# Kernel tuning notes

Hardware: AMD Instinct MI355X
Metric: run time of the kernel (lower is better)

Reference implementation:

```python
import jax, jax.numpy as jnp
import numpy as np

O_IDX = 0  # slot_types.index('O')
X_IDX = 1  # slot_types.index('X')
NUM_INTENTS = 60
NUM_SLOTS = 100
ENCODER_DIM = 300
COS_EPS = 1e-8  # torch CosineSimilarity eps


def _l2_normalize(x):
    n = jnp.linalg.norm(x, axis=-1, keepdims=True)
    return x / jnp.maximum(n, COS_EPS)


def _ce_on_probs(probs, labels):
    # torch cross_entropy applied to (already softmaxed) probs as logits
    logz = jax.nn.logsumexp(probs, axis=-1)
    picked = jnp.take_along_axis(probs, labels[..., None], axis=-1)[..., 0]
    return logz - picked


def setup_inputs() -> dict:
    key = jax.random.key(0)
    ks = jax.random.split(key, 12)
    B, T, H = 128, 128, 768
    inp = {
        'lm_output_1': jax.random.normal(ks[0], (B, T, H), jnp.float32),
        'lm_output_2': jax.random.normal(ks[1], (B, T, H), jnp.float32),
        'intent_labels_1': jax.random.randint(ks[2], (B,), 0, NUM_INTENTS, jnp.int32),
        'intent_labels_2': jax.random.randint(ks[3], (B,), 0, NUM_INTENTS, jnp.int32),
        'slot_labels_1': jax.random.randint(ks[4], (B, T), 0, NUM_SLOTS, jnp.int32),
        'slot_labels_2': jax.random.randint(ks[5], (B, T), 0, NUM_SLOTS, jnp.int32),
        'intent_proto_in': jax.random.normal(ks[6], (NUM_INTENTS, ENCODER_DIM), jnp.float32),
        'intent_count_in': jax.random.randint(ks[7], (NUM_INTENTS,), 1, 50, jnp.int32),
        'slot_proto_in': jax.random.normal(ks[8], (NUM_SLOTS, H), jnp.float32),
        'slot_count_in': jax.random.randint(ks[9], (NUM_SLOTS,), 1, 50, jnp.int32),
        'W_enc': jax.random.normal(ks[10], (ENCODER_DIM, H), jnp.float32) * 0.02,
        'b_enc': jax.random.normal(ks[11], (ENCODER_DIM,), jnp.float32) * 0.02,
        'b_O': jnp.zeros(()),
        'b_X': jnp.zeros(()),
    }
    return inp


def reference(lm_output_1, lm_output_2, intent_labels_1, intent_labels_2,
              slot_labels_1, slot_labels_2, intent_proto_in, intent_count_in,
              slot_proto_in, slot_count_in, W_enc, b_enc, b_O, b_X):
    B, T, H = lm_output_1.shape
    # encoder Linear(hidden -> 300); dropout is identity in eval mode
    enc1 = lm_output_1 @ W_enc.T + b_enc   # [B,T,E]
    enc2 = lm_output_2 @ W_enc.T + b_enc   # [B,T,E] == decoded_2 (use_aae=False)
    slot_proto_enc = slot_proto_in @ W_enc.T + b_enc  # [S,E]

    # ---- prototype update: segment-mean of batch-1 embeddings by class ----
    cls1 = enc1[:, 0, :]  # [B,E]
    i_sum = jax.ops.segment_sum(cls1, intent_labels_1, num_segments=NUM_INTENTS)
    i_cnt = jax.ops.segment_sum(jnp.ones((B,), jnp.float32), intent_labels_1,
                                num_segments=NUM_INTENTS)
    cnt0 = intent_count_in.astype(jnp.float32)
    intent_proto = (cnt0[:, None] * intent_proto_in + i_sum) / (cnt0 + i_cnt)[:, None]
    # faithful to original bug: new count = mean-vector dim = encoder_dim
    intent_count = jnp.full((NUM_INTENTS,), ENCODER_DIM, jnp.int32)

    toks1 = enc1[:, 1:, :].reshape(B * (T - 1), -1)       # [B*(T-1),E]
    slab1 = slot_labels_1[:, 1:].reshape(-1)
    s_sum = jax.ops.segment_sum(toks1, slab1, num_segments=NUM_SLOTS)
    s_cnt = jax.ops.segment_sum(jnp.ones_like(slab1, dtype=jnp.float32), slab1,
                                num_segments=NUM_SLOTS)
    scnt0 = slot_count_in.astype(jnp.float32)
    slot_proto = (scnt0[:, None] * slot_proto_enc + s_sum) / (scnt0 + s_cnt)[:, None]
    slot_count = slot_count_in + s_cnt.astype(jnp.int32)

    # ---- intent: cosine sim to prototypes, softmax, CE on the softmax output ----
    cls2 = enc2[:, 0, :]  # [B,E]
    intent_sim = _l2_normalize(cls2) @ _l2_normalize(intent_proto).T  # [B,I]
    intent_probs = jax.nn.softmax(intent_sim, axis=-1)
    intent_logits = intent_probs[:, None, :]  # [B,1,I]
    intent_loss = jnp.mean(_ce_on_probs(intent_probs, intent_labels_2))

    # ---- slots: cosine sim per token, O/X columns are detached biases ----
    toks2 = enc2[:, 1:, :]  # [B,T-1,E]
    slot_sim = jnp.einsum('btd,sd->bts', _l2_normalize(toks2), _l2_normalize(slot_proto))
    slot_sim = slot_sim.at[:, :, O_IDX].set(jax.lax.stop_gradient(b_O))
    slot_sim = slot_sim.at[:, :, X_IDX].set(jax.lax.stop_gradient(b_X))
    slot_probs = jax.nn.softmax(slot_sim, axis=-1)  # [B,T-1,S]
    slot_logits = slot_probs[:, :, None, :]  # [B,T-1,1,S]
    slot_loss = jnp.mean(_ce_on_probs(slot_probs, slot_labels_2[:, 1:]))

    total_loss = intent_loss + slot_loss
    return (intent_logits, slot_logits, intent_loss, slot_loss, total_loss,
            intent_proto, intent_count, slot_proto, slot_count)
```

## Files before the change

### kernel.cpp

```cpp
#include <hip/hip_runtime.h>
#include <math.h>

#define BB_ 128
#define TT_ 128
#define HDIM 768
#define ED 300
#define NI 60
#define NS 100
#define NTOK 16256

#define WS_ENC1  0
#define WS_ENC2  4915200
#define WS_SPE   9830400
#define WS_ISUM  9860400
#define WS_ICNT  9878400
#define WS_NPTI  9878464
#define WS_NPTS  9896464
#define WS_SSUM  9926464
#define WS_SCNT  9956464
#define WS_PART  9956608
#define WS_LOSSI 13779328
#define WS_LOSSS 13779456

#define O_ILOG   0
#define O_SLOG   7680
#define O_ILOSS  1633280
#define O_SLOSS  1633281
#define O_TLOSS  1633282
#define O_IPROTO 1633283
#define O_ICNT   1651283
#define O_SPROTO 1651343
#define O_SCNT   1681343

typedef __attribute__((ext_vector_type(8))) __bf16 bf16x8;
typedef __attribute__((ext_vector_type(4))) float f32x4;

__device__ __forceinline__ unsigned bf16_rne_u(float x) {
  unsigned u = __float_as_uint(x);
  return (u + 0x7FFFu + ((u >> 16) & 1u)) >> 16;
}
__device__ __forceinline__ void split2(float x, float y, unsigned& hi, unsigned& lo) {
  unsigned hx = bf16_rne_u(x), hy = bf16_rne_u(y);
  float rx = x - __uint_as_float(hx << 16);
  float ry = y - __uint_as_float(hy << 16);
  unsigned lx = bf16_rne_u(rx), ly = bf16_rne_u(ry);
  hi = hx | (hy << 16);
  lo = lx | (ly << 16);
}

__device__ __forceinline__ void gl_lds16(const uint4* g, void* l) {
  __builtin_amdgcn_global_load_lds(
      (const __attribute__((address_space(1))) void*)g,
      (__attribute__((address_space(3))) void*)l, 16, 0, 0);
}

__global__ __launch_bounds__(256) void prep_w(const float* __restrict__ W,
                                              uint4* __restrict__ Wp) {
  int t = blockIdx.x * 256 + threadIdx.x;
  if (t >= 30720) return;
  int ks  = t / 1280;
  int rem = t - ks * 1280;
  int nf  = rem >> 6;
  int c   = (rem >> 2) & 15;
  int kg  = rem & 3;
  int n   = nf * 16 + c;
  int kb  = ks * 32 + kg * 8;
  float4 x0 = make_float4(0.f, 0.f, 0.f, 0.f), x1 = x0;
  if (n < 300) {
    x0 = *(const float4*)(W + (size_t)n * HDIM + kb);
    x1 = *(const float4*)(W + (size_t)n * HDIM + kb + 4);
  }
  unsigned h0, l0, h1, l1, h2, l2, h3, l3;
  split2(x0.x, x0.y, h0, l0); split2(x0.z, x0.w, h1, l1);
  split2(x1.x, x1.y, h2, l2); split2(x1.z, x1.w, h3, l3);
  size_t base = (size_t)ks * 2560;
  int slot = nf * 64 + kg * 16 + c;
  Wp[base + slot]        = make_uint4(h0, h1, h2, h3);
  Wp[base + 1280 + slot] = make_uint4(l0, l1, l2, l3);
}

__global__ __launch_bounds__(512, 4) void gemm_enc_mfma(
    const float* __restrict__ lm1, const float* __restrict__ lm2,
    const float* __restrict__ spin, const uint4* __restrict__ Wp,
    const float* __restrict__ bias, float* __restrict__ ws) {
  __shared__ __align__(16) unsigned char smem[49152];
  int mt = blockIdx.x, m0 = mt * 64;
  const float* src; int srow, mrows;
  if (mt < 256)      { src = lm1;  srow = m0;         mrows = 64; }
  else if (mt < 512) { src = lm2;  srow = m0 - 16384; mrows = 64; }
  else               { src = spin; srow = m0 - 32768; mrows = 100 - srow; }

  int tid = threadIdx.x;
  int l = tid & 63, w = tid >> 6;
  int mf = w & 3, nh = w >> 2;

  int ar = tid >> 3, a8 = tid & 7;
  bool aval = ar < mrows;
  const float* aptr = src + (size_t)(srow + ar) * HDIM + a8 * 4;
  unsigned aw = 40960u + ((unsigned)(ar >> 4) << 10) + ((unsigned)(a8 >> 1) << 8)
              + ((unsigned)(ar & 15) << 4) + ((unsigned)(a8 & 1) << 3);

  const unsigned char* arop = smem + 40960 + (mf << 10) + l * 16;
  const unsigned char* brop = smem + ((nh * 10) << 10) + l * 16;

  f32x4 acc[10];
  #pragma unroll
  for (int i = 0; i < 10; i++) acc[i] = (f32x4)0.f;

  float4 areg = aval ? *(const float4*)(aptr) : make_float4(0.f, 0.f, 0.f, 0.f);

  for (int ks = 0; ks < 24; ks++) {
    {
      unsigned h0, l0, h1, l1;
      split2(areg.x, areg.y, h0, l0);
      split2(areg.z, areg.w, h1, l1);
      *(uint2*)(smem + aw)        = make_uint2(h0, h1);
      *(uint2*)(smem + aw + 4096) = make_uint2(l0, l1);
    }
    {
      const uint4* gp = Wp + (size_t)ks * 2560 + (size_t)(w * 5) * 64 + l;
      #pragma unroll
      for (int i = 0; i < 5; i++)
        gl_lds16(gp + i * 64, smem + (w * 5 + i) * 1024);
    }
    __syncthreads();
    if (ks < 23)
      areg = aval ? *(const float4*)(aptr + (ks + 1) * 32)
                  : make_float4(0.f, 0.f, 0.f, 0.f);
    bf16x8 ah = *(const bf16x8*)(arop);
    bf16x8 al = *(const bf16x8*)(arop + 4096);
    #pragma unroll
    for (int nf = 0; nf < 10; nf++) {
      bf16x8 bh = *(const bf16x8*)(brop + (nf << 10));
      bf16x8 bl = *(const bf16x8*)(brop + (nf << 10) + 20480);
      acc[nf] = __builtin_amdgcn_mfma_f32_16x16x32_bf16(ah, bh, acc[nf], 0, 0, 0);
      acc[nf] = __builtin_amdgcn_mfma_f32_16x16x32_bf16(al, bh, acc[nf], 0, 0, 0);
      acc[nf] = __builtin_amdgcn_mfma_f32_16x16x32_bf16(ah, bl, acc[nf], 0, 0, 0);
    }
    __syncthreads();
  }

  int rbase = (mf << 4) + ((l >> 4) << 2);
  #pragma unroll
  for (int nf = 0; nf < 10; nf++) {
    int n = ((nh * 10 + nf) << 4) + (l & 15);
    if (n >= 300) continue;
    float bn = bias[n];
    #pragma unroll
    for (int r = 0; r < 4; r++) {
      int lr = rbase + r;
      if (lr < mrows) ws[(size_t)(m0 + lr) * ED + n] = acc[nf][r] + bn;
    }
  }
}

__global__ __launch_bounds__(320) void intent_seg(
    const float* __restrict__ enc1, const int* __restrict__ il1,
    float* __restrict__ isum, float* __restrict__ icnt) {
  int seg = blockIdx.x, tid = threadIdx.x;
  if (tid < ED) {
    float a = 0.f;
    for (int b = 0; b < BB_; b++)
      if (il1[b] == seg) a += enc1[(size_t)(b * TT_) * ED + tid];
    isum[seg * ED + tid] = a;
  } else if (tid == ED) {
    float c = 0.f;
    for (int b = 0; b < BB_; b++) c += (il1[b] == seg) ? 1.f : 0.f;
    icnt[seg] = c;
  }
}

__global__ __launch_bounds__(320) void slot_seg_partial(
    const float* __restrict__ enc1, const int* __restrict__ sl1,
    float* __restrict__ part) {
  __shared__ float acc[15050];
  int gid = blockIdx.x;
  int g = gid >> 1, h = gid & 1;
  int tid = threadIdx.x;
  for (int i = tid; i < 15050; i += 320) acc[i] = 0.f;
  __syncthreads();
  int base = h * 50;
  for (int rr = 0; rr < 128; rr++) {
    int j = g * 128 + rr;
    int bb = j / 127, tt = j % 127 + 1;
    int l = sl1[bb * TT_ + tt] - base;
    if (l >= 0 && l < 50) {
      if (tid < ED)       acc[l * ED + tid] += enc1[(size_t)(bb * TT_ + tt) * ED + tid];
      else if (tid == ED) acc[15000 + l] += 1.f;
    }
  }
  __syncthreads();
  float* dst = part + (size_t)gid * 15050;
  for (int i = tid; i < 15050; i += 320) dst[i] = acc[i];
}

__global__ void slot_seg_final(const float* __restrict__ part,
                               float* __restrict__ ssum, float* __restrict__ scnt) {
  int idx = blockIdx.x * 256 + threadIdx.x;
  if (idx < 30000) {
    int S = idx / ED, d = idx % ED;
    int h = S / 50, ls = S % 50;
    float a = 0.f;
    for (int g = 0; g < 127; g++) a += part[(size_t)(g * 2 + h) * 15050 + ls * ED + d];
    ssum[idx] = a;
  } else if (idx < 30100) {
    int S = idx - 30000;
    int h = S / 50, ls = S % 50;
    float a = 0.f;
    for (int g = 0; g < 127; g++) a += part[(size_t)(g * 2 + h) * 15050 + 15000 + ls];
    scnt[S] = a;
  }
}

__global__ void finalize_protos(
    const float* __restrict__ ipin, const int* __restrict__ icin,
    const float* __restrict__ spe, const int* __restrict__ scin,
    const float* __restrict__ isum, const float* __restrict__ icnt,
    const float* __restrict__ ssum, const float* __restrict__ scnt,
    float* __restrict__ dout) {
  int idx = blockIdx.x * 256 + threadIdx.x;
  if (idx < 18000) {
    int i = idx / ED;
    float c0 = (float)icin[i];
    dout[O_IPROTO + idx] = (c0 * ipin[idx] + isum[idx]) / (c0 + icnt[i]);
  } else if (idx < 18060) {
    dout[O_ICNT + (idx - 18000)] = (float)ED;
  } else if (idx < 48060) {
    int k = idx - 18060;
    int s = k / ED;
    float c0 = (float)scin[s];
    dout[O_SPROTO + k] = (c0 * spe[k] + ssum[k]) / (c0 + scnt[s]);
  } else if (idx < 48160) {
    int s = idx - 48060;
    dout[O_SCNT + s] = (float)scin[s] + scnt[s];
  }
}

__global__ __launch_bounds__(320) void norm_protos(
    const float* __restrict__ dout, float* __restrict__ ws) {
  int row = blockIdx.x;
  const float* src; float* dstT; int nrows; int r;
  if (row < NI) { r = row;      src = dout + O_IPROTO + (size_t)r * ED; dstT = ws + WS_NPTI; nrows = NI; }
  else          { r = row - NI; src = dout + O_SPROTO + (size_t)r * ED; dstT = ws + WS_NPTS; nrows = NS; }
  int tid = threadIdx.x;
  float v = (tid < ED) ? src[tid] : 0.f;
  float ss = v * v;
  #pragma unroll
  for (int o = 32; o > 0; o >>= 1) ss += __shfl_xor(ss, o);
  __shared__ float wsum[5];
  if ((tid & 63) == 0) wsum[tid >> 6] = ss;
  __syncthreads();
  float tot = wsum[0] + wsum[1] + wsum[2] + wsum[3] + wsum[4];
  float den = fmaxf(sqrtf(tot), 1e-8f);
  if (tid < ED) dstT[(size_t)tid * nrows + r] = v / den;
}

__global__ __launch_bounds__(64) void intent_head(
    const float* __restrict__ enc2, const float* __restrict__ npTi,
    const int* __restrict__ il2, float* __restrict__ dout,
    float* __restrict__ lossi) {
  int b = blockIdx.x;
  __shared__ float row[ED];
  int tid = threadIdx.x;
  const float* src = enc2 + (size_t)(b * TT_) * ED;
  float ss = 0.f;
  for (int k = tid; k < ED; k += 64) { float v = src[k]; row[k] = v; ss += v * v; }
  #pragma unroll
  for (int o = 32; o > 0; o >>= 1) ss += __shfl_xor(ss, o);
  __syncthreads();
  float den = fmaxf(sqrtf(ss), 1e-8f);
  float dot = 0.f;
  if (tid < NI)
    for (int k = 0; k < ED; k++) dot = fmaf(row[k], npTi[k * NI + tid], dot);
  float sim = dot / den;
  float val = (tid < NI) ? sim : -INFINITY;
  float m = val;
  #pragma unroll
  for (int o = 32; o > 0; o >>= 1) m = fmaxf(m, __shfl_xor(m, o));
  float e = (tid < NI) ? expf(sim - m) : 0.f;
  float s = e;
  #pragma unroll
  for (int o = 32; o > 0; o >>= 1) s += __shfl_xor(s, o);
  float prob = e / s;
  if (tid < NI) dout[O_ILOG + b * NI + tid] = prob;
  float pv = (tid < NI) ? prob : -INFINITY;
  float m2 = pv;
  #pragma unroll
  for (int o = 32; o > 0; o >>= 1) m2 = fmaxf(m2, __shfl_xor(m2, o));
  float e2 = (tid < NI) ? expf(prob - m2) : 0.f;
  float s2 = e2;
  #pragma unroll
  for (int o = 32; o > 0; o >>= 1) s2 += __shfl_xor(s2, o);
  int lbl = il2[b];
  float picked = __shfl(prob, lbl);
  if (tid == 0) lossi[b] = m2 + logf(s2) - picked;
}

__device__ __forceinline__ float bsum128(float v, float* red2) {
  #pragma unroll
  for (int o = 32; o > 0; o >>= 1) v += __shfl_xor(v, o);
  __syncthreads();
  if ((threadIdx.x & 63) == 0) red2[threadIdx.x >> 6] = v;
  __syncthreads();
  return red2[0] + red2[1];
}
__device__ __forceinline__ float bmax128(float v, float* red2) {
  #pragma unroll
  for (int o = 32; o > 0; o >>= 1) v = fmaxf(v, __shfl_xor(v, o));
  __syncthreads();
  if ((threadIdx.x & 63) == 0) red2[threadIdx.x >> 6] = v;
  __syncthreads();
  return fmaxf(red2[0], red2[1]);
}

#define RPB 8
__global__ __launch_bounds__(128) void slot_head(
    const float* __restrict__ enc2, const float* __restrict__ npTs,
    const int* __restrict__ sl2, const float* __restrict__ bO,
    const float* __restrict__ bX, float* __restrict__ dout,
    float* __restrict__ losss) {
  __shared__ float rows[RPB][ED];
  __shared__ float den[RPB];
  __shared__ float red2[2];
  __shared__ float pickedS;
  int tid = threadIdx.x;
  int jb = blockIdx.x * RPB;
  for (int idx = tid; idx < RPB * ED; idx += 128) {
    int r = idx / ED, k = idx % ED;
    int j = jb + r;
    int bb = j / 127, tt = j % 127 + 1;
    rows[r][k] = enc2[(size_t)(bb * TT_ + tt) * ED + k];
  }
  __syncthreads();
  #pragma unroll
  for (int r = 0; r < RPB; r++) {
    float ss = 0.f;
    for (int k = tid; k < ED; k += 128) { float v = rows[r][k]; ss += v * v; }
    ss = bsum128(ss, red2);
    if (tid == 0) den[r] = fmaxf(sqrtf(ss), 1e-8f);
  }
  __syncthreads();
  float acc[RPB] = {};
  int p = tid;
  bool act = p < NS;
  for (int k = 0; k < ED; k += 4) {
    float w0 = act ? npTs[(size_t)(k + 0) * NS + p] : 0.f;
    float w1 = act ? npTs[(size_t)(k + 1) * NS + p] : 0.f;
    float w2 = act ? npTs[(size_t)(k + 2) * NS + p] : 0.f;
    float w3 = act ? npTs[(size_t)(k + 3) * NS + p] : 0.f;
    #pragma unroll
    for (int r = 0; r < RPB; r++) {
      float4 rv = *(const float4*)&rows[r][k];
      acc[r] = fmaf(rv.x, w0, acc[r]);
      acc[r] = fmaf(rv.y, w1, acc[r]);
      acc[r] = fmaf(rv.z, w2, acc[r]);
      acc[r] = fmaf(rv.w, w3, acc[r]);
    }
  }
  float vO = *bO, vX = *bX;
  for (int r = 0; r < RPB; r++) {
    int j = jb + r;
    int bb = j / 127, tt = j % 127 + 1;
    float sim = acc[r] / den[r];
    if (p == 0) sim = vO;
    if (p == 1) sim = vX;
    float val = act ? sim : -INFINITY;
    float m = bmax128(val, red2);
    float e = act ? expf(sim - m) : 0.f;
    float s = bsum128(e, red2);
    float prob = e / s;
    if (act) dout[O_SLOG + (size_t)j * NS + p] = prob;
    float pv = act ? prob : -INFINITY;
    float m2 = bmax128(pv, red2);
    int lbl = sl2[bb * TT_ + tt];
    if (p == lbl) pickedS = prob;
    float e2 = act ? expf(prob - m2) : 0.f;
    float s2 = bsum128(e2, red2);
    if (tid == 0) losss[j] = m2 + logf(s2) - pickedS;
  }
}

__global__ __launch_bounds__(256) void loss_final(
    const float* __restrict__ li, const float* __restrict__ lsv,
    float* __restrict__ dout) {
  __shared__ float red[256];
  int tid = threadIdx.x;
  float a = (tid < BB_) ? li[tid] : 0.f;
  red[tid] = a;
  __syncthreads();
  for (int o = 128; o > 0; o >>= 1) {
    if (tid < o) red[tid] += red[tid + o];
    __syncthreads();
  }
  float il = red[0];
  __syncthreads();
  float bsum = 0.f;
  for (int i = tid; i < NTOK; i += 256) bsum += lsv[i];
  red[tid] = bsum;
  __syncthreads();
  for (int o = 128; o > 0; o >>= 1) {
    if (tid < o) red[tid] += red[tid + o];
    __syncthreads();
  }
  if (tid == 0) {
    float ilm = il / 128.f;
    float slm = red[0] / 16256.f;
    dout[O_ILOSS] = ilm;
    dout[O_SLOSS] = slm;
    dout[O_TLOSS] = ilm + slm;
  }
}

extern "C" void kernel_launch(void* const* d_in, const int* in_sizes, int n_in,
                              void* d_out, int out_size, void* d_ws, size_t ws_size,
                              hipStream_t stream) {
  const float* lm1  = (const float*)d_in[0];
  const float* lm2  = (const float*)d_in[1];
  const int*   il1  = (const int*)d_in[2];
  const int*   il2  = (const int*)d_in[3];
  const int*   sl1  = (const int*)d_in[4];
  const int*   sl2  = (const int*)d_in[5];
  const float* ipin = (const float*)d_in[6];
  const int*   icin = (const int*)d_in[7];
  const float* spin = (const float*)d_in[8];
  const int*   scin = (const int*)d_in[9];
  const float* W    = (const float*)d_in[10];
  const float* benc = (const float*)d_in[11];
  const float* bO   = (const float*)d_in[12];
  const float* bX   = (const float*)d_in[13];
  float* out = (float*)d_out;
  float* ws  = (float*)d_ws;
  uint4* Wp  = (uint4*)(ws + WS_PART);

  prep_w<<<120, 256, 0, stream>>>(W, Wp);
  gemm_enc_mfma<<<514, 512, 0, stream>>>(lm1, lm2, spin, Wp, benc, ws);
  intent_seg<<<60, 320, 0, stream>>>(ws + WS_ENC1, il1, ws + WS_ISUM, ws + WS_ICNT);
  slot_seg_partial<<<254, 320, 0, stream>>>(ws + WS_ENC1, sl1, ws + WS_PART);
  slot_seg_final<<<118, 256, 0, stream>>>(ws + WS_PART, ws + WS_SSUM, ws + WS_SCNT);
  finalize_protos<<<189, 256, 0, stream>>>(ipin, icin, ws + WS_SPE, scin,
                                           ws + WS_ISUM, ws + WS_ICNT,
                                           ws + WS_SSUM, ws + WS_SCNT, out);
  norm_protos<<<160, 320, 0, stream>>>(out, ws);
  intent_head<<<128, 64, 0, stream>>>(ws + WS_ENC2, ws + WS_NPTI, il2, out, ws + WS_LOSSI);
  slot_head<<<2032, 128, 0, stream>>>(ws + WS_ENC2, ws + WS_NPTS, sl2, bO, bX, out, ws + WS_LOSSS);
  loss_final<<<1, 256, 0, stream>>>(ws + WS_LOSSI, ws + WS_LOSSS, out);
}
```

Before: 369.5 us.

## Compute slot cosine similarities with split-bf16 MFMA instead of scalar FMA

Replaces the scalar per-thread slot_head with an MFMA kernel. Normalised token rows are split into bf16 hi/lo pairs and multiplied against pre-packed, split normalised slot prototypes using three 16x16x32 bf16 MFMAs per tile, giving near-fp32 accuracy. A new prep_npts kernel packs the prototype matrix into the MFMA-friendly layout, reusing the WS_PART workspace. The softmax and CE reductions now run per 16-lane group with shuffles, replacing block-wide syncthreads reductions, and each block handles 32 tokens. The cost is an extra launch and a small precision loss from the bf16x3 decomposition.

```diff
diff --git a/kernel.cpp b/kernel.cpp
--- a/kernel.cpp
+++ b/kernel.cpp
@@ -255,6 +255,30 @@
   if (tid < ED) dstT[(size_t)tid * nrows + r] = v / den;
 }
 
+__global__ __launch_bounds__(256) void prep_npts(const float* __restrict__ npTs,
+                                                 uint4* __restrict__ Wq) {
+  int t = blockIdx.x * 256 + threadIdx.x;
+  if (t >= 4480) return;
+  int ks  = t / 448;
+  int rem = t - ks * 448;
+  int nf  = rem >> 6;
+  int c   = (rem >> 2) & 15;
+  int kg  = rem & 3;
+  int s   = nf * 16 + c;
+  int kb  = ks * 32 + kg * 8;
+  float v[8];
+  #pragma unroll
+  for (int i = 0; i < 8; i++)
+    v[i] = (s < NS && (kb + i) < ED) ? npTs[(size_t)(kb + i) * NS + s] : 0.f;
+  unsigned h0, l0, h1, l1, h2, l2, h3, l3;
+  split2(v[0], v[1], h0, l0); split2(v[2], v[3], h1, l1);
+  split2(v[4], v[5], h2, l2); split2(v[6], v[7], h3, l3);
+  size_t base = (size_t)ks * 896;
+  int slot = nf * 64 + kg * 16 + c;
+  Wq[base + slot]       = make_uint4(h0, h1, h2, h3);
+  Wq[base + 448 + slot] = make_uint4(l0, l1, l2, l3);
+}
+
 __global__ __launch_bounds__(64) void intent_head(
     const float* __restrict__ enc2, const float* __restrict__ npTi,
     const int* __restrict__ il2, float* __restrict__ dout,
@@ -296,87 +320,149 @@
   if (tid == 0) lossi[b] = m2 + logf(s2) - picked;
 }
 
-__device__ __forceinline__ float bsum128(float v, float* red2) {
-  #pragma unroll
-  for (int o = 32; o > 0; o >>= 1) v += __shfl_xor(v, o);
-  __syncthreads();
-  if ((threadIdx.x & 63) == 0) red2[threadIdx.x >> 6] = v;
-  __syncthreads();
-  return red2[0] + red2[1];
-}
-__device__ __forceinline__ float bmax128(float v, float* red2) {
-  #pragma unroll
-  for (int o = 32; o > 0; o >>= 1) v = fmaxf(v, __shfl_xor(v, o));
-  __syncthreads();
-  if ((threadIdx.x & 63) == 0) red2[threadIdx.x >> 6] = v;
-  __syncthreads();
-  return fmaxf(red2[0], red2[1]);
-}
-
-#define RPB 8
-__global__ __launch_bounds__(128) void slot_head(
-    const float* __restrict__ enc2, const float* __restrict__ npTs,
+__global__ __launch_bounds__(128) void slot_head_mfma(
+    const float* __restrict__ enc2, const uint4* __restrict__ Wq,
     const int* __restrict__ sl2, const float* __restrict__ bO,
     const float* __restrict__ bX, float* __restrict__ dout,
     float* __restrict__ losss) {
-  __shared__ float rows[RPB][ED];
-  __shared__ float den[RPB];
-  __shared__ float red2[2];
-  __shared__ float pickedS;
+  __shared__ __align__(16) unsigned char smem[18560];
+  float* invd = (float*)(smem + 18432);
   int tid = threadIdx.x;
-  int jb = blockIdx.x * RPB;
-  for (int idx = tid; idx < RPB * ED; idx += 128) {
-    int r = idx / ED, k = idx % ED;
-    int j = jb + r;
-    int bb = j / 127, tt = j % 127 + 1;
-    rows[r][k] = enc2[(size_t)(bb * TT_ + tt) * ED + k];
-  }
-  __syncthreads();
-  #pragma unroll
-  for (int r = 0; r < RPB; r++) {
-    float ss = 0.f;
-    for (int k = tid; k < ED; k += 128) { float v = rows[r][k]; ss += v * v; }
-    ss = bsum128(ss, red2);
-    if (tid == 0) den[r] = fmaxf(sqrtf(ss), 1e-8f);
-  }
-  __syncthreads();
-  float acc[RPB] = {};
-  int p = tid;
-  bool act = p < NS;
-  for (int k = 0; k < ED; k += 4) {
-    float w0 = act ? npTs[(size_t)(k + 0) * NS + p] : 0.f;
-    float w1 = act ? npTs[(size_t)(k + 1) * NS + p] : 0.f;
-    float w2 = act ? npTs[(size_t)(k + 2) * NS + p] : 0.f;
-    float w3 = act ? npTs[(size_t)(k + 3) * NS + p] : 0.f;
-    #pragma unroll
-    for (int r = 0; r < RPB; r++) {
-      float4 rv = *(const float4*)&rows[r][k];
-      acc[r] = fmaf(rv.x, w0, acc[r]);
-      acc[r] = fmaf(rv.y, w1, acc[r]);
-      acc[r] = fmaf(rv.z, w2, acc[r]);
-      acc[r] = fmaf(rv.w, w3, acc[r]);
-    }
-  }
+  int l = tid & 63, w = tid >> 6;
+  int blk = blockIdx.x;
+  int j0 = blk * 32;
+
+  int nrow = tid >> 2, nq = tid & 3;
+  int jn = j0 + nrow;
+  int tokn = (jn / 127) * TT_ + (jn % 127) + 1;
+  const float* nsrc = enc2 + (size_t)tokn * ED + nq * 75;
+  float ss = 0.f;
+  for (int i = 0; i < 75; i++) { float v = nsrc[i]; ss = fmaf(v, v, ss); }
+  ss += __shfl_xor(ss, 1);
+  ss += __shfl_xor(ss, 2);
+  if (nq == 0) invd[nrow] = 1.f / fmaxf(sqrtf(ss), 1e-8f);
+  __syncthreads();
+
+  const float* asrc = enc2 + (size_t)tokn * ED;
+  unsigned awr = 14336u + ((unsigned)(nrow >> 4) << 10) + ((unsigned)nq << 8)
+               + ((unsigned)(nrow & 15) << 4);
+  float ainv = invd[nrow];
+
+  const unsigned char* arop = smem + 14336 + (w << 10) + l * 16;
+  const unsigned char* brop = smem + l * 16;
+
+  f32x4 acc[7];
+  #pragma unroll
+  for (int i = 0; i < 7; i++) acc[i] = (f32x4)0.f;
+
+  for (int ks = 0; ks < 10; ks++) {
+    {
+      int k0 = ks * 32 + nq * 8;
+      float4 v0 = (k0 <= 296) ? *(const float4*)(asrc + k0)
+                              : make_float4(0.f, 0.f, 0.f, 0.f);
+      float4 v1 = (k0 + 4 <= 296) ? *(const float4*)(asrc + k0 + 4)
+                                  : make_float4(0.f, 0.f, 0.f, 0.f);
+      v0.x *= ainv; v0.y *= ainv; v0.z *= ainv; v0.w *= ainv;
+      v1.x *= ainv; v1.y *= ainv; v1.z *= ainv; v1.w *= ainv;
+      unsigned h0, l0, h1, l1, h2, l2, h3, l3;
+      split2(v0.x, v0.y, h0, l0); split2(v0.z, v0.w, h1, l1);
+      split2(v1.x, v1.y, h2, l2); split2(v1.z, v1.w, h3, l3);
+      *(uint4*)(smem + awr)        = make_uint4(h0, h1, h2, h3);
+      *(uint4*)(smem + awr + 2048) = make_uint4(l0, l1, l2, l3);
+    }
+    {
+      const uint4* gp = Wq + (size_t)ks * 896;
+      #pragma unroll
+      for (int i = 0; i < 7; i++) {
+        int c1 = i * 2 + w;
+        gl_lds16(gp + c1 * 64 + l, smem + c1 * 1024);
+      }
+    }
+    __syncthreads();
+    bf16x8 ah = *(const bf16x8*)(arop);
+    bf16x8 al = *(const bf16x8*)(arop + 2048);
+    #pragma unroll
+    for (int nf = 0; nf < 7; nf++) {
+      bf16x8 bh = *(const bf16x8*)(brop + (nf << 10));
+      bf16x8 bl = *(const bf16x8*)(brop + (nf << 10) + 7168);
+      acc[nf] = __builtin_amdgcn_mfma_f32_16x16x32_bf16(ah, bh, acc[nf], 0, 0, 0);
+      acc[nf] = __builtin_amdgcn_mfma_f32_16x16x32_bf16(al, bh, acc[nf], 0, 0, 0);
+      acc[nf] = __builtin_amdgcn_mfma_f32_16x16x32_bf16(ah, bl, acc[nf], 0, 0, 0);
+    }
+    __syncthreads();
+  }
+
   float vO = *bO, vX = *bX;
-  for (int r = 0; r < RPB; r++) {
-    int j = jb + r;
-    int bb = j / 127, tt = j % 127 + 1;
-    float sim = acc[r] / den[r];
-    if (p == 0) sim = vO;
-    if (p == 1) sim = vX;
-    float val = act ? sim : -INFINITY;
-    float m = bmax128(val, red2);
-    float e = act ? expf(sim - m) : 0.f;
-    float s = bsum128(e, red2);
-    float prob = e / s;
-    if (act) dout[O_SLOG + (size_t)j * NS + p] = prob;
-    float pv = act ? prob : -INFINITY;
-    float m2 = bmax128(pv, red2);
-    int lbl = sl2[bb * TT_ + tt];
-    if (p == lbl) pickedS = prob;
-    float e2 = act ? expf(prob - m2) : 0.f;
-    float s2 = bsum128(e2, red2);
-    if (tid == 0) losss[j] = m2 + logf(s2) - pickedS;
+  int c16 = l & 15, g = l >> 4;
+  #pragma unroll
+  for (int r = 0; r < 4; r++) {
+    int j = j0 + w * 16 + g * 4 + r;
+    int tok = (j / 127) * TT_ + (j % 127) + 1;
+    int lbl = sl2[tok];
+    float sim[7];
+    #pragma unroll
+    for (int nf = 0; nf < 7; nf++) sim[nf] = acc[nf][r];
+    if (c16 == 0) sim[0] = vO;
+    if (c16 == 1) sim[0] = vX;
+    float mx = -INFINITY;
+    #pragma unroll
+    for (int nf = 0; nf < 7; nf++) {
+      bool valid = (nf < 6) || (c16 < 4);
+      float v = valid ? sim[nf] : -INFINITY;
+      mx = fmaxf(mx, v);
+    }
+    mx = fmaxf(mx, __shfl_xor(mx, 1));
+    mx = fmaxf(mx, __shfl_xor(mx, 2));
+    mx = fmaxf(mx, __shfl_xor(mx, 4));
+    mx = fmaxf(mx, __shfl_xor(mx, 8));
+    float e[7], s = 0.f;
+    #pragma unroll
+    for (int nf = 0; nf < 7; nf++) {
+      bool valid = (nf < 6) || (c16 < 4);
+      e[nf] = valid ? expf(sim[nf] - mx) : 0.f;
+      s += e[nf];
+    }
+    s += __shfl_xor(s, 1);
+    s += __shfl_xor(s, 2);
+    s += __shfl_xor(s, 4);
+    s += __shfl_xor(s, 8);
+    float p[7];
+    #pragma unroll
+    for (int nf = 0; nf < 7; nf++) p[nf] = e[nf] / s;
+    #pragma unroll
+    for (int nf = 0; nf < 7; nf++) {
+      int col = nf * 16 + c16;
+      if (col < NS) dout[O_SLOG + (size_t)j * NS + col] = p[nf];
+    }
+    float m2 = -INFINITY;
+    #pragma unroll
+    for (int nf = 0; nf < 7; nf++) {
+      bool valid = (nf < 6) || (c16 < 4);
+      m2 = fmaxf(m2, valid ? p[nf] : -INFINITY);
+    }
+    m2 = fmaxf(m2, __shfl_xor(m2, 1));
+    m2 = fmaxf(m2, __shfl_xor(m2, 2));
+    m2 = fmaxf(m2, __shfl_xor(m2, 4));
+    m2 = fmaxf(m2, __shfl_xor(m2, 8));
+    float s2 = 0.f, pick = 0.f;
+    #pragma unroll
+    for (int nf = 0; nf < 7; nf++) {
+      bool valid = (nf < 6) || (c16 < 4);
+      if (valid) {
+        s2 += expf(p[nf] - m2);
+        int col = nf * 16 + c16;
+        pick += (col == lbl) ? p[nf] : 0.f;
+      }
+    }
+    s2 += __shfl_xor(s2, 1);
+    s2 += __shfl_xor(s2, 2);
+    s2 += __shfl_xor(s2, 4);
+    s2 += __shfl_xor(s2, 8);
+    pick += __shfl_xor(pick, 1);
+    pick += __shfl_xor(pick, 2);
+    pick += __shfl_xor(pick, 4);
+    pick += __shfl_xor(pick, 8);
+    if (c16 == 0) losss[j] = m2 + logf(s2) - pick;
   }
 }
 
@@ -431,6 +517,7 @@
   float* out = (float*)d_out;
   float* ws  = (float*)d_ws;
   uint4* Wp  = (uint4*)(ws + WS_PART);
+  uint4* Wq  = (uint4*)(ws + WS_PART);
 
   prep_w<<<120, 256, 0, stream>>>(W, Wp);
   gemm_enc_mfma<<<514, 512, 0, stream>>>(lm1, lm2, spin, Wp, benc, ws);
@@ -442,6 +529,7 @@
                                            ws + WS_SSUM, ws + WS_SCNT, out);
   norm_protos<<<160, 320, 0, stream>>>(out, ws);
   intent_head<<<128, 64, 0, stream>>>(ws + WS_ENC2, ws + WS_NPTI, il2, out, ws + WS_LOSSI);
-  slot_head<<<2032, 128, 0, stream>>>(ws + WS_ENC2, ws + WS_NPTS, sl2, bO, bX, out, ws + WS_LOSSS);
+  prep_npts<<<18, 256, 0, stream>>>(ws + WS_NPTS, Wq);
+  slot_head_mfma<<<508, 128, 0, stream>>>(ws + WS_ENC2, Wq, sl2, bO, bX, out, ws + WS_LOSSS);
   loss_final<<<1, 256, 0, stream>>>(ws + WS_LOSSI, ws + WS_LOSSS, out);
 }
```

Measured after the change: 335.3 us. 9.3% less time.
